# Kernel optimization log

Measured on AMD Instinct MI355X. Metric: run time of the kernel, lower is better.

The kernel has to match this reference:

```python
import jax, jax.numpy as jnp
import numpy as np

B, S, D = 1, 4096, 1024
H, G = 16, 4
DK = D // H            # 64, per-head dim
HKV = H // G           # 4 KV heads
DKV = D // G           # 256, KV projection width
SCALE = 1.0 / np.sqrt(np.float32(DK))


def setup_inputs() -> dict:
    key = jax.random.key(0)
    ks = jax.random.split(key, 10)
    std = 0.02
    return {
        "x": jax.random.normal(ks[0], (B, S, D), jnp.float32),
        "mask": jax.random.bernoulli(ks[1], 0.1, (B, 1, S)),  # True = masked out
        "Wq": jax.random.normal(ks[2], (D, D), jnp.float32) * std,
        "bq": jnp.zeros((D,), jnp.float32),
        "Wk": jax.random.normal(ks[3], (D, DKV), jnp.float32) * std,
        "bk": jnp.zeros((DKV,), jnp.float32),
        "Wv": jax.random.normal(ks[4], (D, DKV), jnp.float32) * std,
        "bv": jnp.zeros((DKV,), jnp.float32),
        "Wo": jax.random.normal(ks[5], (D, D), jnp.float32) * std,
        "bo": jnp.zeros((D,), jnp.float32),
    }


def reference(x, mask, Wq, bq, Wk, bk, Wv, bv, Wo, bo):
    b, s, _ = x.shape
    # projections
    q = (x @ Wq + bq).reshape(b, s, H, DK).transpose(0, 2, 1, 3)      # [B,H,S,DK]
    k = (x @ Wk + bk).reshape(b, s, HKV, DK).transpose(0, 2, 1, 3)    # [B,HKV,S,DK]
    v = (x @ Wv + bv).reshape(b, s, HKV, DK).transpose(0, 2, 1, 3)    # [B,HKV,S,DK]
    # expand KV heads: head h = kv_head * G + g (matches torch expand+reshape)
    k = jnp.repeat(k, G, axis=1)                                       # [B,H,S,DK]
    v = jnp.repeat(v, G, axis=1)                                       # [B,H,S,DK]
    scores = jnp.einsum("bhsd,bhtd->bhst", q, k) * SCALE              # [B,H,S,S]
    neg_inf = jnp.finfo(scores.dtype).min
    scores = jnp.where(mask[:, None, :, :], neg_inf, scores)           # mask: [B,1,1,S]
    attn = jax.nn.softmax(scores, axis=-1)
    out = jnp.einsum("bhst,bhtd->bhsd", attn, v)                      # [B,H,S,DK]
    out = out.transpose(0, 2, 1, 3).reshape(b, s, D)
    return out @ Wo + bo
```

## Files before the change

### kernel.cpp

```cpp
#include <hip/hip_runtime.h>
#include <cstdint>
#include <cstddef>

#define S_LEN 4096
#define DMODEL 1024
#define NHEADS 16
#define HDK 64
#define DKV 256
#define NTOT 1536
#define QSCALE 0.18033688011112042f

typedef __bf16 bf16;
typedef __bf16 bf16x8 __attribute__((ext_vector_type(8)));
typedef float f32x4 __attribute__((ext_vector_type(4)));

typedef __attribute__((address_space(3))) void lds_void;
typedef const __attribute__((address_space(1))) void gbl_void;

__device__ __forceinline__ void gload16(const void* g, void* l) {
  __builtin_amdgcn_global_load_lds((gbl_void*)g, (lds_void*)l, 16, 0, 0);
}

__global__ __launch_bounds__(256) void prep(
    const float* __restrict__ x, const int* __restrict__ mask,
    const float* __restrict__ Wq, const float* __restrict__ Wk,
    const float* __restrict__ Wv, const float* __restrict__ Wo,
    bf16* __restrict__ xb, float* __restrict__ mkf, bf16* __restrict__ mkb,
    bf16* __restrict__ Wqt, bf16* __restrict__ Wkt,
    bf16* __restrict__ Wvt, bf16* __restrict__ Wot) {
  const int z = blockIdx.z;
  if (z < 4) {
    const float* src;
    bf16* dst;
    int C;
    switch (z) {
      case 0: src = Wq; dst = Wqt; C = DMODEL; break;
      case 1: src = Wk; dst = Wkt; C = DKV; break;
      case 2: src = Wv; dst = Wvt; C = DKV; break;
      default: src = Wo; dst = Wot; C = DMODEL; break;
    }
    const int c0 = blockIdx.x * 32;
    if (c0 >= C) return;
    __shared__ float tile[32][33];
    const int tx = threadIdx.x & 31;
    const int ty = threadIdx.x >> 5;
    const int r0 = blockIdx.y * 32;
#pragma unroll
    for (int i = 0; i < 4; i++)
      tile[ty + i * 8][tx] = src[(size_t)(r0 + ty + i * 8) * C + c0 + tx];
    __syncthreads();
#pragma unroll
    for (int i = 0; i < 4; i++)
      dst[(size_t)(c0 + ty + i * 8) * DMODEL + r0 + tx] = (bf16)tile[tx][ty + i * 8];
  } else {
    const int b = blockIdx.y * 32 + blockIdx.x;
    const int half = z - 4;
    const int i = ((half * 1024 + b) * 256 + (int)threadIdx.x) * 8;
    float4 a = *(const float4*)(x + i);
    float4 c = *(const float4*)(x + i + 4);
    bf16 o[8] = {(bf16)a.x, (bf16)a.y, (bf16)a.z, (bf16)a.w,
                 (bf16)c.x, (bf16)c.y, (bf16)c.z, (bf16)c.w};
    *(uint4*)(xb + i) = *(uint4*)o;
    if (half == 1 && b < 2) {
      const int mi = (b * 256 + (int)threadIdx.x) * 8;
#pragma unroll
      for (int j = 0; j < 8; j++) {
        float keep = mask[mi + j] ? 0.0f : 1.0f;
        mkf[mi + j] = keep;
        mkb[mi + j] = (bf16)keep;
      }
    }
  }
}

template <int QKV>
__global__ __launch_bounds__(256) void gemm_ld(
    const bf16* __restrict__ A, const bf16* __restrict__ Bt, int M, int N, int K,
    int NT,
    const float* __restrict__ bq, const float* __restrict__ bk,
    const float* __restrict__ bv, const float* __restrict__ mkf,
    bf16* __restrict__ Qb, bf16* __restrict__ Kb, bf16* __restrict__ Vtb,
    const float* __restrict__ bo, float* __restrict__ Co) {
  __shared__ bf16 As[64 * 64];
  __shared__ bf16 Bs[128 * 64];
  const int t = threadIdx.x;
  const int lane = t & 63;
  const int wave = t >> 6;

  const int bid = blockIdx.x;
  const int xcd = bid & 7;
  const int local = bid >> 3;
  const int m_local = local / NT;
  const int ntile = local - m_local * NT;
  const int mchunk = (M >> 6) >> 3;
  const int m0 = (xcd * mchunk + m_local) * 64;
  const int n0 = ntile * 128;

  const int wm = (wave >> 1) * 32;
  const int wn = (wave & 1) * 64;
  const int lr = lane & 15;
  const int quad = lane >> 4;

  const int sr = lane >> 3;
  const int sc = ((lane & 7) ^ (lane >> 3)) * 8;

  f32x4 acc[2][4] = {};

  for (int k0 = 0; k0 < K; k0 += 64) {
    __syncthreads();
#pragma unroll
    for (int j = 0; j < 2; j++) {
      const int rbase = wave * 16 + j * 8;
      gload16(A + (size_t)(m0 + rbase + sr) * K + k0 + sc, &As[rbase * 64]);
    }
#pragma unroll
    for (int j = 0; j < 4; j++) {
      const int rbase = wave * 32 + j * 8;
      gload16(Bt + (size_t)(n0 + rbase + sr) * K + k0 + sc, &Bs[rbase * 64]);
    }
    __syncthreads();
#pragma unroll
    for (int kh2 = 0; kh2 < 2; kh2++) {
      const int fo = ((kh2 * 4 + quad) ^ (lr & 7)) * 8;
      bf16x8 af[2], bfr[4];
#pragma unroll
      for (int mt = 0; mt < 2; mt++)
        af[mt] = *(const bf16x8*)(&As[(wm + mt * 16 + lr) * 64 + fo]);
#pragma unroll
      for (int nt = 0; nt < 4; nt++)
        bfr[nt] = *(const bf16x8*)(&Bs[(wn + nt * 16 + lr) * 64 + fo]);
#pragma unroll
      for (int mt = 0; mt < 2; mt++)
#pragma unroll
        for (int nt = 0; nt < 4; nt++)
          acc[mt][nt] = __builtin_amdgcn_mfma_f32_16x16x32_bf16(af[mt], bfr[nt], acc[mt][nt], 0, 0, 0);
    }
  }

#pragma unroll
  for (int nt = 0; nt < 4; nt++) {
    const int n = n0 + wn + nt * 16 + lr;
    if (QKV) {
      if (n < DMODEL) {
        const float b = bq[n];
#pragma unroll
        for (int mt = 0; mt < 2; mt++)
#pragma unroll
          for (int r = 0; r < 4; r++) {
            const int m = m0 + wm + mt * 16 + quad * 4 + r;
            Qb[(size_t)m * DMODEL + n] = (bf16)((acc[mt][nt][r] + b) * QSCALE);
          }
      } else if (n < DMODEL + DKV) {
        const float b = bk[n - DMODEL];
#pragma unroll
        for (int mt = 0; mt < 2; mt++)
#pragma unroll
          for (int r = 0; r < 4; r++) {
            const int m = m0 + wm + mt * 16 + quad * 4 + r;
            Kb[(size_t)m * DKV + (n - DMODEL)] = (bf16)(acc[mt][nt][r] + b);
          }
      } else {
        const float b = bv[n - DMODEL - DKV];
#pragma unroll
        for (int mt = 0; mt < 2; mt++)
#pragma unroll
          for (int r = 0; r < 4; r++) {
            const int m = m0 + wm + mt * 16 + quad * 4 + r;
            Vtb[(size_t)(n - DMODEL - DKV) * S_LEN + m] = (bf16)((acc[mt][nt][r] + b) * mkf[m]);
          }
      }
    } else {
      const float b = bo[n];
#pragma unroll
      for (int mt = 0; mt < 2; mt++)
#pragma unroll
        for (int r = 0; r < 4; r++) {
          const int m = m0 + wm + mt * 16 + quad * 4 + r;
          Co[(size_t)m * N + n] = acc[mt][nt][r] + b;
        }
    }
  }
}

__global__ __launch_bounds__(256) void flash_attn(
    const bf16* __restrict__ Q, const bf16* __restrict__ K,
    const bf16* __restrict__ Vt, const bf16* __restrict__ mkb,
    bf16* __restrict__ O) {
  const int h = blockIdx.y;
  const int kvh = h >> 2;
  const int q0 = blockIdx.x * 128;
  const int t = threadIdx.x;
  const int lane = t & 63;
  const int wave = t >> 6;
  const int lr = lane & 15;
  const int quad = lane >> 4;

  __shared__ bf16 Ks[2][64 * 64];
  __shared__ bf16 Vs[2][64 * 64];
  __shared__ bf16 Ps[4][32][36];

  bf16x8 aq[2][2];
#pragma unroll
  for (int qt = 0; qt < 2; qt++) {
    const int qrow = q0 + wave * 32 + qt * 16 + lr;
    aq[qt][0] = *(const bf16x8*)(Q + (size_t)qrow * DMODEL + h * HDK + quad * 8);
    aq[qt][1] = *(const bf16x8*)(Q + (size_t)qrow * DMODEL + h * HDK + 32 + quad * 8);
  }

  const bf16* Kg = K + kvh * HDK;
  const bf16* Vg = Vt + (size_t)kvh * HDK * S_LEN;
  const int krl = lane >> 3;
  const int kgc = ((lane & 7) ^ krl) * 8;

#pragma unroll
  for (int j = 0; j < 2; j++) {
    const int rb = wave * 16 + j * 8;
    gload16(Kg + (size_t)(rb + krl) * DKV + kgc, &Ks[0][rb * 64]);
  }
#pragma unroll
  for (int j = 0; j < 2; j++) {
    const int rb = wave * 16 + j * 8;
    gload16(Vg + (size_t)(rb + krl) * S_LEN + kgc, &Vs[0][rb * 64]);
  }

  f32x4 o_acc[2][4] = {};
  f32x4 l_acc[2] = {};
  int buf = 0;

  for (int kv0 = 0; kv0 < S_LEN; kv0 += 64) {
    __syncthreads();
    const int kvn = kv0 + 64;
    if (kvn < S_LEN) {
      const int nb = buf ^ 1;
#pragma unroll
      for (int j = 0; j < 2; j++) {
        const int rb = wave * 16 + j * 8;
        gload16(Kg + (size_t)(kvn + rb + krl) * DKV + kgc, &Ks[nb][rb * 64]);
      }
#pragma unroll
      for (int j = 0; j < 2; j++) {
        const int rb = wave * 16 + j * 8;
        gload16(Vg + (size_t)(rb + krl) * S_LEN + kvn + kgc, &Vs[nb][rb * 64]);
      }
    }
    const bf16* Ksb = Ks[buf];
    const bf16* Vsb = Vs[buf];

#pragma unroll
    for (int kc = 0; kc < 2; kc++) {
      bf16x8 ak[2][2];
#pragma unroll
      for (int ntl = 0; ntl < 2; ntl++) {
        const int krow = kc * 32 + ntl * 16 + lr;
        ak[ntl][0] = *(const bf16x8*)(&Ksb[krow * 64 + (quad ^ (lr & 7)) * 8]);
        ak[ntl][1] = *(const bf16x8*)(&Ksb[krow * 64 + ((4 + quad) ^ (lr & 7)) * 8]);
      }
#pragma unroll
      for (int qt = 0; qt < 2; qt++) {
#pragma unroll
        for (int ntl = 0; ntl < 2; ntl++) {
          f32x4 s = {};
          s = __builtin_amdgcn_mfma_f32_16x16x32_bf16(ak[ntl][0], aq[qt][0], s, 0, 0, 0);
          s = __builtin_amdgcn_mfma_f32_16x16x32_bf16(ak[ntl][1], aq[qt][1], s, 0, 0, 0);
          bf16 p4[4];
#pragma unroll
          for (int r = 0; r < 4; r++) p4[r] = (bf16)__builtin_amdgcn_exp2f(s[r]);
          *(uint2*)(&Ps[wave][qt * 16 + lr][ntl * 16 + quad * 4]) = *(uint2*)p4;
        }
      }
      bf16x8 bvf[4];
#pragma unroll
      for (int ntv = 0; ntv < 4; ntv++) {
        const int vrow = ntv * 16 + lr;
        bvf[ntv] = *(const bf16x8*)(&Vsb[vrow * 64 + ((kc * 4 + quad) ^ (lr & 7)) * 8]);
      }
      const bf16x8 mkfv = *(const bf16x8*)(mkb + kv0 + kc * 32 + quad * 8);
#pragma unroll
      for (int qt = 0; qt < 2; qt++) {
        bf16x8 ap = *(const bf16x8*)(&Ps[wave][qt * 16 + lr][quad * 8]);
#pragma unroll
        for (int ntv = 0; ntv < 4; ntv++)
          o_acc[qt][ntv] = __builtin_amdgcn_mfma_f32_16x16x32_bf16(ap, bvf[ntv], o_acc[qt][ntv], 0, 0, 0);
        l_acc[qt] = __builtin_amdgcn_mfma_f32_16x16x32_bf16(ap, mkfv, l_acc[qt], 0, 0, 0);
      }
    }
    buf ^= 1;
  }

#pragma unroll
  for (int qt = 0; qt < 2; qt++) {
#pragma unroll
    for (int ntv = 0; ntv < 4; ntv++) {
#pragma unroll
      for (int r = 0; r < 4; r++) {
        const int row = q0 + wave * 32 + qt * 16 + quad * 4 + r;
        O[(size_t)row * DMODEL + h * HDK + ntv * 16 + lr] =
            (bf16)(o_acc[qt][ntv][r] / l_acc[qt][r]);
      }
    }
  }
}

extern "C" void kernel_launch(void* const* d_in, const int* in_sizes, int n_in,
                              void* d_out, int out_size, void* d_ws, size_t ws_size,
                              hipStream_t stream) {
  const float* x = (const float*)d_in[0];
  const int* mask = (const int*)d_in[1];
  const float* Wq = (const float*)d_in[2];
  const float* bq = (const float*)d_in[3];
  const float* Wk = (const float*)d_in[4];
  const float* bk = (const float*)d_in[5];
  const float* Wv = (const float*)d_in[6];
  const float* bv = (const float*)d_in[7];
  const float* Wo = (const float*)d_in[8];
  const float* bo = (const float*)d_in[9];
  float* out = (float*)d_out;

  char* w = (char*)d_ws;
  bf16* xb  = (bf16*)w; w += (size_t)S_LEN * DMODEL * 2;
  bf16* Wqt = (bf16*)w; w += (size_t)DMODEL * DMODEL * 2;
  bf16* Wkt = (bf16*)w; w += (size_t)DKV * DMODEL * 2;
  bf16* Wvt = (bf16*)w; w += (size_t)DKV * DMODEL * 2;
  bf16* Wot = (bf16*)w; w += (size_t)DMODEL * DMODEL * 2;
  bf16* Qb  = (bf16*)w; w += (size_t)S_LEN * DMODEL * 2;
  bf16* Kb  = (bf16*)w; w += (size_t)S_LEN * DKV * 2;
  bf16* Vtb = (bf16*)w; w += (size_t)DKV * S_LEN * 2;
  bf16* Ob  = (bf16*)w; w += (size_t)S_LEN * DMODEL * 2;
  float* mkf = (float*)w; w += (size_t)S_LEN * 4;
  bf16* mkb = (bf16*)w; w += (size_t)S_LEN * 2;

  prep<<<dim3(32, 32, 6), 256, 0, stream>>>(
      x, mask, Wq, Wk, Wv, Wo, xb, mkf, mkb, Wqt, Wkt, Wvt, Wot);

  gemm_ld<1><<<dim3((S_LEN / 64) * (NTOT / 128)), 256, 0, stream>>>(
      xb, Wqt, S_LEN, NTOT, DMODEL, NTOT / 128, bq, bk, bv, mkf, Qb, Kb, Vtb,
      nullptr, nullptr);

  flash_attn<<<dim3(S_LEN / 128, NHEADS), 256, 0, stream>>>(Qb, Kb, Vtb, mkb, Ob);

  gemm_ld<0><<<dim3((S_LEN / 64) * (DMODEL / 128)), 256, 0, stream>>>(
      Ob, Wot, S_LEN, DMODEL, DMODEL, DMODEL / 128, nullptr, nullptr, nullptr,
      nullptr, nullptr, nullptr, nullptr, bo, out);
}
```

Before: 218.5 us.

## Split each KV tile across two wave groups in flash attention and reduce partials

```diff
diff --git a/kernel.cpp b/kernel.cpp
--- a/kernel.cpp
+++ b/kernel.cpp
@@ -182,7 +182,7 @@
   }
 }
 
-__global__ __launch_bounds__(256) void flash_attn(
+__global__ __launch_bounds__(512) void flash_attn(
     const bf16* __restrict__ Q, const bf16* __restrict__ K,
     const bf16* __restrict__ Vt, const bf16* __restrict__ mkb,
     bf16* __restrict__ O) {
@@ -192,17 +192,20 @@
   const int t = threadIdx.x;
   const int lane = t & 63;
   const int wave = t >> 6;
+  const int w4 = wave & 3;
+  const int kc = wave >> 2;
   const int lr = lane & 15;
   const int quad = lane >> 4;
 
-  __shared__ bf16 Ks[2][64 * 64];
-  __shared__ bf16 Vs[2][64 * 64];
-  __shared__ bf16 Ps[4][32][36];
+  __shared__ __align__(16) char smem_raw[51200];
+  bf16* KsBase = (bf16*)smem_raw;
+  bf16* VsBase = (bf16*)(smem_raw + 16384);
+  bf16 (*Ps)[32][36] = (bf16(*)[32][36])(smem_raw + 32768);
 
   bf16x8 aq[2][2];
 #pragma unroll
   for (int qt = 0; qt < 2; qt++) {
-    const int qrow = q0 + wave * 32 + qt * 16 + lr;
+    const int qrow = q0 + w4 * 32 + qt * 16 + lr;
     aq[qt][0] = *(const bf16x8*)(Q + (size_t)qrow * DMODEL + h * HDK + quad * 8);
     aq[qt][1] = *(const bf16x8*)(Q + (size_t)qrow * DMODEL + h * HDK + 32 + quad * 8);
   }
@@ -212,15 +215,18 @@
   const int krl = lane >> 3;
   const int kgc = ((lane & 7) ^ krl) * 8;
 
-#pragma unroll
-  for (int j = 0; j < 2; j++) {
-    const int rb = wave * 16 + j * 8;
-    gload16(Kg + (size_t)(rb + krl) * DKV + kgc, &Ks[0][rb * 64]);
-  }
-#pragma unroll
-  for (int j = 0; j < 2; j++) {
-    const int rb = wave * 16 + j * 8;
-    gload16(Vg + (size_t)(rb + krl) * S_LEN + kgc, &Vs[0][rb * 64]);
+  if (wave < 4) {
+#pragma unroll
+    for (int j = 0; j < 2; j++) {
+      const int rb = w4 * 16 + j * 8;
+      gload16(Kg + (size_t)(rb + krl) * DKV + kgc, KsBase + rb * 64);
+    }
+  } else {
+#pragma unroll
+    for (int j = 0; j < 2; j++) {
+      const int rb = w4 * 16 + j * 8;
+      gload16(Vg + (size_t)(rb + krl) * S_LEN + kgc, VsBase + rb * 64);
+    }
   }
 
   f32x4 o_acc[2][4] = {};
@@ -232,71 +238,93 @@
     const int kvn = kv0 + 64;
     if (kvn < S_LEN) {
       const int nb = buf ^ 1;
-#pragma unroll
-      for (int j = 0; j < 2; j++) {
-        const int rb = wave * 16 + j * 8;
-        gload16(Kg + (size_t)(kvn + rb + krl) * DKV + kgc, &Ks[nb][rb * 64]);
+      if (wave < 4) {
+#pragma unroll
+        for (int j = 0; j < 2; j++) {
+          const int rb = w4 * 16 + j * 8;
+          gload16(Kg + (size_t)(kvn + rb + krl) * DKV + kgc, KsBase + nb * 4096 + rb * 64);
+        }
+      } else {
+#pragma unroll
+        for (int j = 0; j < 2; j++) {
+          const int rb = w4 * 16 + j * 8;
+          gload16(Vg + (size_t)(rb + krl) * S_LEN + kvn + kgc, VsBase + nb * 4096 + rb * 64);
+        }
       }
-#pragma unroll
-      for (int j = 0; j < 2; j++) {
-        const int rb = wave * 16 + j * 8;
-        gload16(Vg + (size_t)(rb + krl) * S_LEN + kvn + kgc, &Vs[nb][rb * 64]);
+    }
+    const bf16* Ksb = KsBase + buf * 4096;
+    const bf16* Vsb = VsBase + buf * 4096;
+
+    bf16x8 ak[2][2];
+#pragma unroll
+    for (int ntl = 0; ntl < 2; ntl++) {
+      const int krow = kc * 32 + ntl * 16 + lr;
+      ak[ntl][0] = *(const bf16x8*)(&Ksb[krow * 64 + (quad ^ (lr & 7)) * 8]);
+      ak[ntl][1] = *(const bf16x8*)(&Ksb[krow * 64 + ((4 + quad) ^ (lr & 7)) * 8]);
+    }
+#pragma unroll
+    for (int qt = 0; qt < 2; qt++) {
+#pragma unroll
+      for (int ntl = 0; ntl < 2; ntl++) {
+        f32x4 s = {};
+        s = __builtin_amdgcn_mfma_f32_16x16x32_bf16(ak[ntl][0], aq[qt][0], s, 0, 0, 0);
+        s = __builtin_amdgcn_mfma_f32_16x16x32_bf16(ak[ntl][1], aq[qt][1], s, 0, 0, 0);
+        bf16 p4[4];
+#pragma unroll
+        for (int r = 0; r < 4; r++) p4[r] = (bf16)__builtin_amdgcn_exp2f(s[r]);
+        *(uint2*)(&Ps[wave][qt * 16 + lr][ntl * 16 + quad * 4]) = *(uint2*)p4;
       }
     }
-    const bf16* Ksb = Ks[buf];
-    const bf16* Vsb = Vs[buf];
-
-#pragma unroll
-    for (int kc = 0; kc < 2; kc++) {
-      bf16x8 ak[2][2];
-#pragma unroll
-      for (int ntl = 0; ntl < 2; ntl++) {
-        const int krow = kc * 32 + ntl * 16 + lr;
-        ak[ntl][0] = *(const bf16x8*)(&Ksb[krow * 64 + (quad ^ (lr & 7)) * 8]);
-        ak[ntl][1] = *(const bf16x8*)(&Ksb[krow * 64 + ((4 + quad) ^ (lr & 7)) * 8]);
-      }
-#pragma unroll
-      for (int qt = 0; qt < 2; qt++) {
-#pragma unroll
-        for (int ntl = 0; ntl < 2; ntl++) {
-          f32x4 s = {};
-          s = __builtin_amdgcn_mfma_f32_16x16x32_bf16(ak[ntl][0], aq[qt][0], s, 0, 0, 0);
-          s = __builtin_amdgcn_mfma_f32_16x16x32_bf16(ak[ntl][1], aq[qt][1], s, 0, 0, 0);
-          bf16 p4[4];
-#pragma unroll
-          for (int r = 0; r < 4; r++) p4[r] = (bf16)__builtin_amdgcn_exp2f(s[r]);
-          *(uint2*)(&Ps[wave][qt * 16 + lr][ntl * 16 + quad * 4]) = *(uint2*)p4;
-        }
-      }
-      bf16x8 bvf[4];
-#pragma unroll
-      for (int ntv = 0; ntv < 4; ntv++) {
-        const int vrow = ntv * 16 + lr;
-        bvf[ntv] = *(const bf16x8*)(&Vsb[vrow * 64 + ((kc * 4 + quad) ^ (lr & 7)) * 8]);
-      }
-      const bf16x8 mkfv = *(const bf16x8*)(mkb + kv0 + kc * 32 + quad * 8);
-#pragma unroll
-      for (int qt = 0; qt < 2; qt++) {
-        bf16x8 ap = *(const bf16x8*)(&Ps[wave][qt * 16 + lr][quad * 8]);
-#pragma unroll
-        for (int ntv = 0; ntv < 4; ntv++)
-          o_acc[qt][ntv] = __builtin_amdgcn_mfma_f32_16x16x32_bf16(ap, bvf[ntv], o_acc[qt][ntv], 0, 0, 0);
-        l_acc[qt] = __builtin_amdgcn_mfma_f32_16x16x32_bf16(ap, mkfv, l_acc[qt], 0, 0, 0);
-      }
+    bf16x8 bvf[4];
+#pragma unroll
+    for (int ntv = 0; ntv < 4; ntv++) {
+      const int vrow = ntv * 16 + lr;
+      bvf[ntv] = *(const bf16x8*)(&Vsb[vrow * 64 + ((kc * 4 + quad) ^ (lr & 7)) * 8]);
+    }
+    const bf16x8 mkfv = *(const bf16x8*)(mkb + kv0 + kc * 32 + quad * 8);
+#pragma unroll
+    for (int qt = 0; qt < 2; qt++) {
+      bf16x8 ap = *(const bf16x8*)(&Ps[wave][qt * 16 + lr][quad * 8]);
+#pragma unroll
+      for (int ntv = 0; ntv < 4; ntv++)
+        o_acc[qt][ntv] = __builtin_amdgcn_mfma_f32_16x16x32_bf16(ap, bvf[ntv], o_acc[qt][ntv], 0, 0, 0);
+      l_acc[qt] = __builtin_amdgcn_mfma_f32_16x16x32_bf16(ap, mkfv, l_acc[qt], 0, 0, 0);
     }
     buf ^= 1;
   }
 
-#pragma unroll
-  for (int qt = 0; qt < 2; qt++) {
-#pragma unroll
-    for (int ntv = 0; ntv < 4; ntv++) {
-#pragma unroll
-      for (int r = 0; r < 4; r++) {
-        const int row = q0 + wave * 32 + qt * 16 + quad * 4 + r;
-        O[(size_t)row * DMODEL + h * HDK + ntv * 16 + lr] =
-            (bf16)(o_acc[qt][ntv][r] / l_acc[qt][r]);
-      }
+  float* Oc = (float*)smem_raw;
+  float* Lc = (float*)(smem_raw + 32768);
+  __syncthreads();
+  if (wave >= 4) {
+#pragma unroll
+    for (int qt = 0; qt < 2; qt++) {
+#pragma unroll
+      for (int ntv = 0; ntv < 4; ntv++)
+#pragma unroll
+        for (int r = 0; r < 4; r++) {
+          const int rl = w4 * 32 + qt * 16 + quad * 4 + r;
+          Oc[rl * 64 + ntv * 16 + lr] = o_acc[qt][ntv][r];
+        }
+      if (lr == 0)
+#pragma unroll
+        for (int r = 0; r < 4; r++)
+          Lc[w4 * 32 + qt * 16 + quad * 4 + r] = l_acc[qt][r];
+    }
+  }
+  __syncthreads();
+  if (wave < 4) {
+#pragma unroll
+    for (int qt = 0; qt < 2; qt++) {
+#pragma unroll
+      for (int ntv = 0; ntv < 4; ntv++)
+#pragma unroll
+        for (int r = 0; r < 4; r++) {
+          const int rl = w4 * 32 + qt * 16 + quad * 4 + r;
+          const float ov = o_acc[qt][ntv][r] + Oc[rl * 64 + ntv * 16 + lr];
+          const float lv = l_acc[qt][r] + Lc[rl];
+          O[(size_t)(q0 + rl) * DMODEL + h * HDK + ntv * 16 + lr] = (bf16)(ov / lv);
+        }
     }
   }
 }
@@ -336,7 +364,7 @@
       xb, Wqt, S_LEN, NTOT, DMODEL, NTOT / 128, bq, bk, bv, mkf, Qb, Kb, Vtb,
       nullptr, nullptr);
 
-  flash_attn<<<dim3(S_LEN / 128, NHEADS), 256, 0, stream>>>(Qb, Kb, Vtb, mkb, Ob);
+  flash_attn<<<dim3(S_LEN / 128, NHEADS), 512, 0, stream>>>(Qb, Kb, Vtb, mkb, Ob);
 
   gemm_ld<0><<<dim3((S_LEN / 64) * (DMODEL / 128)), 256, 0, stream>>>(
       Ob, Wot, S_LEN, DMODEL, DMODEL, DMODEL / 128, nullptr, nullptr, nullptr,
```

Result: slower. 240.5 us (+10.1%).

## Triple-buffer K/V tiles in flash attention with partial vmcnt waits

Applied to the files above, without the earlier changes.

```diff
diff --git a/kernel.cpp b/kernel.cpp
--- a/kernel.cpp
+++ b/kernel.cpp
@@ -195,8 +195,8 @@
   const int lr = lane & 15;
   const int quad = lane >> 4;
 
-  __shared__ bf16 Ks[2][64 * 64];
-  __shared__ bf16 Vs[2][64 * 64];
+  __shared__ bf16 Ks[3][64 * 64];
+  __shared__ bf16 Vs[3][64 * 64];
   __shared__ bf16 Ps[4][32][36];
 
   bf16x8 aq[2][2];
@@ -213,38 +213,47 @@
   const int kgc = ((lane & 7) ^ krl) * 8;
 
 #pragma unroll
-  for (int j = 0; j < 2; j++) {
-    const int rb = wave * 16 + j * 8;
-    gload16(Kg + (size_t)(rb + krl) * DKV + kgc, &Ks[0][rb * 64]);
-  }
-#pragma unroll
-  for (int j = 0; j < 2; j++) {
-    const int rb = wave * 16 + j * 8;
-    gload16(Vg + (size_t)(rb + krl) * S_LEN + kgc, &Vs[0][rb * 64]);
+  for (int tt = 0; tt < 2; tt++) {
+#pragma unroll
+    for (int j = 0; j < 2; j++) {
+      const int rb = wave * 16 + j * 8;
+      gload16(Kg + (size_t)(tt * 64 + rb + krl) * DKV + kgc, &Ks[tt][rb * 64]);
+    }
+#pragma unroll
+    for (int j = 0; j < 2; j++) {
+      const int rb = wave * 16 + j * 8;
+      gload16(Vg + (size_t)(rb + krl) * S_LEN + tt * 64 + kgc, &Vs[tt][rb * 64]);
+    }
   }
 
   f32x4 o_acc[2][4] = {};
   f32x4 l_acc[2] = {};
-  int buf = 0;
+  int bi = 0;
 
   for (int kv0 = 0; kv0 < S_LEN; kv0 += 64) {
-    __syncthreads();
-    const int kvn = kv0 + 64;
-    if (kvn < S_LEN) {
-      const int nb = buf ^ 1;
+    if (kv0 + 64 < S_LEN) {
+      asm volatile("s_waitcnt vmcnt(4)" ::: "memory");
+    } else {
+      asm volatile("s_waitcnt vmcnt(0)" ::: "memory");
+    }
+    __builtin_amdgcn_s_barrier();
+
+    const int kvp = kv0 + 128;
+    if (kvp < S_LEN) {
+      const int nb = bi + 2 >= 3 ? bi - 1 : bi + 2;
 #pragma unroll
       for (int j = 0; j < 2; j++) {
         const int rb = wave * 16 + j * 8;
-        gload16(Kg + (size_t)(kvn + rb + krl) * DKV + kgc, &Ks[nb][rb * 64]);
+        gload16(Kg + (size_t)(kvp + rb + krl) * DKV + kgc, &Ks[nb][rb * 64]);
       }
 #pragma unroll
       for (int j = 0; j < 2; j++) {
         const int rb = wave * 16 + j * 8;
-        gload16(Vg + (size_t)(rb + krl) * S_LEN + kvn + kgc, &Vs[nb][rb * 64]);
-      }
-    }
-    const bf16* Ksb = Ks[buf];
-    const bf16* Vsb = Vs[buf];
+        gload16(Vg + (size_t)(rb + krl) * S_LEN + kvp + kgc, &Vs[nb][rb * 64]);
+      }
+    }
+    const bf16* Ksb = Ks[bi];
+    const bf16* Vsb = Vs[bi];
 
 #pragma unroll
     for (int kc = 0; kc < 2; kc++) {
@@ -284,7 +293,7 @@
         l_acc[qt] = __builtin_amdgcn_mfma_f32_16x16x32_bf16(ap, mkfv, l_acc[qt], 0, 0, 0);
       }
     }
-    buf ^= 1;
+    bi = bi == 2 ? 0 : bi + 1;
   }
 
 #pragma unroll
```

Result: no change. 219.6 us (+0.5%).
